# Kernel tuning notes

Hardware: AMD Instinct MI355X
Metric: run time of the kernel (lower is better)

Reference implementation:

```python
import jax, jax.numpy as jnp
import numpy as np


def setup_inputs() -> dict:
    key = jax.random.key(0)
    k1, k2, k3, k4 = jax.random.split(key, 4)
    B, T, IN, D = 32, 256, 64, 128
    x = jax.random.normal(k1, (B, T, IN), dtype=jnp.float32)
    h0 = jnp.zeros((B, D), dtype=jnp.float32)
    Wx = jax.random.normal(k2, (IN, D), dtype=jnp.float32) * 0.01
    Wgate = jax.random.normal(k3, (D, D), dtype=jnp.float32) * 0.01
    Wh = jax.random.normal(k4, (D, D), dtype=jnp.float32) * 0.01
    return {"x": x, "h0": h0, "Wx": Wx, "Wgate": Wgate, "Wh": Wh}


def reference(x, h0, Wx, Wgate, Wh):
    # x: (B, T, in_dim); h0: (B, dim); returns (h_final, y, hidden_grads, dh_dWh)
    def step_single(h_r, x_r):
        # per-sample gated update: h_r (dim,), x_r (in_dim,)
        pre = x_r @ Wx + h_r @ Wh
        a = jax.nn.gelu(pre, approximate=False)  # torch GELU() is the exact erf variant
        g = jax.nn.sigmoid(a @ Wgate)
        hn = g * h_r + (1.0 - g)
        return hn, hn

    # per-step, per-sample Jacobian d h_new / d h  (mirrors vmap(jacrev(..., argnums=1)))
    jac_batched = jax.vmap(jax.jacrev(step_single, argnums=0, has_aux=True))

    def body(h, x_t):  # h: (B, dim), x_t: (B, in_dim)
        jac, h_new = jac_batched(h, x_t)  # jac: (B, dim, dim)
        return h_new, (h_new, jac)

    xt = jnp.swapaxes(x, 0, 1)  # (T, B, in_dim)
    h_final, (ys, jacs) = jax.lax.scan(body, h0, xt)
    y = jnp.swapaxes(ys, 0, 1)  # (B, T, dim)

    # last-step Jacobian wrt Wh, evaluated with the post-update h (as in the torch code)
    x_last = x[:, -1, :]

    def f_wh(Wh_):
        pre = x_last @ Wx + h_final @ Wh_
        a = jax.nn.gelu(pre, approximate=False)
        g = jax.nn.sigmoid(a @ Wgate)
        return g * h_final + (1.0 - g)

    dh_dWh = jax.jacrev(f_wh)(Wh)  # (B, dim, dim, dim)
    return (h_final, y, jacs, dh_dWh)
```

## Files before the change

kernel.cpp:

```cpp
#include <hip/hip_runtime.h>


#define JACOFF 1052672L
#define DHWOFF 135270400L

typedef __attribute__((ext_vector_type(8))) short frag_ab;
typedef __attribute__((ext_vector_type(4))) float frag_cd;

__device__ __forceinline__ short f2bf(float f) {
    unsigned u = __builtin_bit_cast(unsigned, f);
    unsigned r = (u + 0x7fffu + ((u >> 16) & 1u)) >> 16;
    return (short)r;
}

__device__ __forceinline__ void wg_barrier() {
    asm volatile("s_waitcnt lgkmcnt(0)\n\ts_barrier" ::: "memory");
}

__device__ __forceinline__ float row_reduce16(float x) {
    int t;
    t = __builtin_amdgcn_mov_dpp(__builtin_bit_cast(int, x), 0x128, 0xF, 0xF, true);
    x += __builtin_bit_cast(float, t);
    t = __builtin_amdgcn_mov_dpp(__builtin_bit_cast(int, x), 0x124, 0xF, 0xF, true);
    x += __builtin_bit_cast(float, t);
    t = __builtin_amdgcn_mov_dpp(__builtin_bit_cast(int, x), 0x4E, 0xF, 0xF, true);
    x += __builtin_bit_cast(float, t);
    t = __builtin_amdgcn_mov_dpp(__builtin_bit_cast(int, x), 0xB1, 0xF, 0xF, true);
    x += __builtin_bit_cast(float, t);
    return x;
}

__device__ __forceinline__ void gelu_pair(float pre, float& a, float& dval) {
    const float inv_sqrt2   = 0.70710678118654752f;
    const float inv_sqrt2pi = 0.39894228040143268f;
    float ex2 = __expf(-0.5f * pre * pre);
    float az  = fabsf(pre) * inv_sqrt2;
    float t   = 1.0f / (1.0f + 0.3275911f * az);
    float poly = ((((1.061405429f * t - 1.453152027f) * t + 1.421413741f) * t
                   - 0.284496736f) * t + 0.254829592f) * t;
    float erf_abs = 1.0f - poly * ex2;
    float erf_z = (pre < 0.f) ? -erf_abs : erf_abs;
    float cdf = 0.5f * (1.0f + erf_z);
    a = pre * cdf;
    dval = cdf + pre * inv_sqrt2pi * ex2;
}

__global__ __launch_bounds__(256) void prep_xw_kernel(
    const float* __restrict__ Wh, const float* __restrict__ Wg,
    const float* __restrict__ x, const float* __restrict__ Wx,
    float* __restrict__ whT, float* __restrict__ wgT, float* __restrict__ xw)
{
    int blk = blockIdx.x;
    int tid = threadIdx.x;
    if (blk < 128) {
        int idx = blk * 256 + tid;
        if (idx < 16384) {
            int k = idx >> 7, i = idx & 127;
            whT[i * 128 + k] = Wh[idx];
        } else {
            int r = idx - 16384;
            int k = r >> 7, i = r & 127;
            wgT[i * 128 + k] = Wg[r];
        }
        return;
    }
    __shared__ float xs[2][64];
    int sub = tid >> 7;
    int bt = (blk - 128) * 2 + sub;
    int i = tid & 127;
    if (i < 64) xs[sub][i] = x[bt * 64 + i];
    __syncthreads();
    float acc = 0.f;
#pragma unroll
    for (int m = 0; m < 64; ++m)
        acc += xs[sub][m] * Wx[m * 128 + i];
    xw[bt * 128 + i] = acc;
}

__global__ __launch_bounds__(512, 1) void scan_pk_kernel(
    const float* __restrict__ xw, const float* __restrict__ h0,
    const float* __restrict__ whT, const float* __restrict__ wgT,
    const float* __restrict__ Wgate, const float* __restrict__ Wh,
    float* __restrict__ out,
    short* __restrict__ Abf, float* __restrict__ wgv, float* __restrict__ wc,
    float* __restrict__ wdF, float* __restrict__ wuF, float* __restrict__ whF,
    short* __restrict__ PT)
{
    int tid = threadIdx.x;
    if (blockIdx.x >= 32) {
        int c = (blockIdx.x - 32) * 32 + (tid >> 4);
        int k0 = (tid & 15) * 8;
        int i = c >> 7, j = c & 127;
        short v[8];
#pragma unroll
        for (int m = 0; m < 8; ++m) {
            float wg = Wgate[(k0 + m) * 128 + i];
            float wh = Wh[j * 128 + k0 + m];
            v[m] = f2bf(wg * wh);
        }
        *(frag_ab*)(PT + (long)c * 128 + k0) = *(frag_ab*)v;
        return;
    }

    const int b = blockIdx.x;
    const int og = tid >> 4;
    const int kg = tid & 15;
    const int mm = kg & 3;
    const int iw = og * 4 + kg;
    const bool wlane = (kg < 4);

    __shared__ float hbuf[2][128];
    __shared__ float abuf[128];

    float wh[4][8], wgc[4][8];
#pragma unroll
    for (int m = 0; m < 4; ++m) {
        const float* whr = whT + (og * 4 + m) * 128 + kg * 8;
        const float* wgr = wgT + (og * 4 + m) * 128 + kg * 8;
        float4 a4 = *(const float4*)(whr);
        float4 b4 = *(const float4*)(whr + 4);
        wh[m][0] = a4.x; wh[m][1] = a4.y; wh[m][2] = a4.z; wh[m][3] = a4.w;
        wh[m][4] = b4.x; wh[m][5] = b4.y; wh[m][6] = b4.z; wh[m][7] = b4.w;
        float4 c4 = *(const float4*)(wgr);
        float4 d4 = *(const float4*)(wgr + 4);
        wgc[m][0] = c4.x; wgc[m][1] = c4.y; wgc[m][2] = c4.z; wgc[m][3] = c4.w;
        wgc[m][4] = d4.x; wgc[m][5] = d4.y; wgc[m][6] = d4.z; wgc[m][7] = d4.w;
    }
    if (wlane) hbuf[0][iw] = h0[b * 128 + iw];
    __syncthreads();

    float4 xwv4 = *(const float4*)(xw + (b * 256 + 0) * 128 + og * 4);
    float4 xw14 = *(const float4*)(xw + (b * 256 + 1) * 128 + og * 4);

    for (int t = 0; t < 256; ++t) {
        int p = t & 1;
        int tn = (t < 254) ? t + 2 : 255;
        float4 xw24 = *(const float4*)(xw + (b * 256 + tn) * 128 + og * 4);

        float h8[8];
        {
            const float* hb = &hbuf[p][kg * 8];
            float4 a4 = *(const float4*)(hb);
            float4 b4 = *(const float4*)(hb + 4);
            h8[0] = a4.x; h8[1] = a4.y; h8[2] = a4.z; h8[3] = a4.w;
            h8[4] = b4.x; h8[5] = b4.y; h8[6] = b4.z; h8[7] = b4.w;
        }
        float s0 = 0.f, s1 = 0.f, s2 = 0.f, s3 = 0.f;
#pragma unroll
        for (int kk = 0; kk < 8; ++kk) {
            s0 += h8[kk] * wh[0][kk];
            s1 += h8[kk] * wh[1][kk];
            s2 += h8[kk] * wh[2][kk];
            s3 += h8[kk] * wh[3][kk];
        }
        s0 = row_reduce16(s0); s1 = row_reduce16(s1);
        s2 = row_reduce16(s2); s3 = row_reduce16(s3);

        float pre = (mm == 0) ? (xwv4.x + s0) : (mm == 1) ? (xwv4.y + s1)
                  : (mm == 2) ? (xwv4.z + s2) : (xwv4.w + s3);
        float a, dval;
        gelu_pair(pre, a, dval);

        long tb = (long)(t * 32 + b) * 128 + iw;
        if (wlane) {
            Abf[tb] = f2bf(dval);
            abuf[iw] = a;
        }
        wg_barrier();

        float a8[8];
        {
            const float* ab = &abuf[kg * 8];
            float4 a4 = *(const float4*)(ab);
            float4 b4 = *(const float4*)(ab + 4);
            a8[0] = a4.x; a8[1] = a4.y; a8[2] = a4.z; a8[3] = a4.w;
            a8[4] = b4.x; a8[5] = b4.y; a8[6] = b4.z; a8[7] = b4.w;
        }
        float r0 = 0.f, r1 = 0.f, r2 = 0.f, r3 = 0.f;
#pragma unroll
        for (int kk = 0; kk < 8; ++kk) {
            r0 += a8[kk] * wgc[0][kk];
            r1 += a8[kk] * wgc[1][kk];
            r2 += a8[kk] * wgc[2][kk];
            r3 += a8[kk] * wgc[3][kk];
        }
        r0 = row_reduce16(r0); r1 = row_reduce16(r1);
        r2 = row_reduce16(r2); r3 = row_reduce16(r3);
        float r = (mm == 0) ? r0 : (mm == 1) ? r1 : (mm == 2) ? r2 : r3;

        float g = 1.0f / (1.0f + __expf(-r));
        float hp = hbuf[p][og * 4 + mm];
        float c = (hp - 1.0f) * g * (1.0f - g);
        float hn = g * hp + 1.0f - g;
        if (wlane) {
            hbuf[p ^ 1][iw] = hn;
            wgv[tb] = g;
            wc[tb] = c;
            out[4096 + (b * 256 + t) * 128 + iw] = hn;
        }
        xwv4 = xw14; xw14 = xw24;
        wg_barrier();
    }

    float hfin = hbuf[0][og * 4 + mm];
    if (wlane) {
        out[b * 128 + iw] = hbuf[0][iw];
        whF[b * 128 + iw] = hbuf[0][iw];
    }

    {
        float h8[8];
        {
            const float* hb = &hbuf[0][kg * 8];
            float4 a4 = *(const float4*)(hb);
            float4 b4 = *(const float4*)(hb + 4);
            h8[0] = a4.x; h8[1] = a4.y; h8[2] = a4.z; h8[3] = a4.w;
            h8[4] = b4.x; h8[5] = b4.y; h8[6] = b4.z; h8[7] = b4.w;
        }
        float s0 = 0.f, s1 = 0.f, s2 = 0.f, s3 = 0.f;
#pragma unroll
        for (int kk = 0; kk < 8; ++kk) {
            s0 += h8[kk] * wh[0][kk];
            s1 += h8[kk] * wh[1][kk];
            s2 += h8[kk] * wh[2][kk];
            s3 += h8[kk] * wh[3][kk];
        }
        s0 = row_reduce16(s0); s1 = row_reduce16(s1);
        s2 = row_reduce16(s2); s3 = row_reduce16(s3);
        float pre = (mm == 0) ? (xwv4.x + s0) : (mm == 1) ? (xwv4.y + s1)
                  : (mm == 2) ? (xwv4.z + s2) : (xwv4.w + s3);
        float a, dval;
        gelu_pair(pre, a, dval);
        if (wlane) {
            wdF[b * 128 + iw] = dval;
            abuf[iw] = a;
        }
        __syncthreads();
        float a8[8];
        {
            const float* ab = &abuf[kg * 8];
            float4 a4 = *(const float4*)(ab);
            float4 b4 = *(const float4*)(ab + 4);
            a8[0] = a4.x; a8[1] = a4.y; a8[2] = a4.z; a8[3] = a4.w;
            a8[4] = b4.x; a8[5] = b4.y; a8[6] = b4.z; a8[7] = b4.w;
        }
        float r0 = 0.f, r1 = 0.f, r2 = 0.f, r3 = 0.f;
#pragma unroll
        for (int kk = 0; kk < 8; ++kk) {
            r0 += a8[kk] * wgc[0][kk];
            r1 += a8[kk] * wgc[1][kk];
            r2 += a8[kk] * wgc[2][kk];
            r3 += a8[kk] * wgc[3][kk];
        }
        r0 = row_reduce16(r0); r1 = row_reduce16(r1);
        r2 = row_reduce16(r2); r3 = row_reduce16(r3);
        float r = (mm == 0) ? r0 : (mm == 1) ? r1 : (mm == 2) ? r2 : r3;
        float g = 1.0f / (1.0f + __expf(-r));
        if (wlane) wuF[b * 128 + iw] = (hfin - 1.0f) * g * (1.0f - g);
    }
}

__global__ __launch_bounds__(256) void jacmm_dhdw_kernel(
    const short* __restrict__ Abf,
    const short* __restrict__ PT,
    const float* __restrict__ wgv,
    const float* __restrict__ wc,
    const float* __restrict__ Wgate,
    const float* __restrict__ dF, const float* __restrict__ uF, const float* __restrict__ hF,
    float* __restrict__ out)
{
    int bx = blockIdx.x;
    int tid = threadIdx.x;
    int grp = bx / 3, rem = bx % 3;

    __shared__ float cstage[64 * 132];

    if (rem == 2) {
        __shared__ float hs[128], dsh[128];
        int b = grp >> 7, i = grp & 127;
        if (tid < 128) {
            hs[tid] = hF[b * 128 + tid];
            dsh[tid] = dF[b * 128 + tid];
        }
        __syncthreads();
        float u = uF[b * 128 + i];
        int q0 = (tid & 31) * 4, p0 = (tid >> 5) * 16;
        float w0 = u * dsh[q0 + 0] * Wgate[(q0 + 0) * 128 + i];
        float w1 = u * dsh[q0 + 1] * Wgate[(q0 + 1) * 128 + i];
        float w2 = u * dsh[q0 + 2] * Wgate[(q0 + 2) * 128 + i];
        float w3 = u * dsh[q0 + 3] * Wgate[(q0 + 3) * 128 + i];
        float* dst = out + DHWOFF + (long)grp * 16384;
#pragma unroll
        for (int pp = 0; pp < 16; ++pp) {
            float hp = hs[p0 + pp];
            frag_cd v4; v4[0] = hp * w0; v4[1] = hp * w1; v4[2] = hp * w2; v4[3] = hp * w3;
            __builtin_nontemporal_store(v4, (frag_cd*)(dst + (p0 + pp) * 128 + q0));
        }
        return;
    }

    int jb = grp * 2 + rem;
    int rb = jb & 63;
    int cb = jb >> 6;

    const short* Ag = Abf + (long)rb * (128 * 128);
    const short* Bg = PT + (long)cb * (128 * 128);

    int w = tid >> 6;
    int lane = tid & 63;
    int wr = w >> 1;
    int wcol = w & 1;
    int lrow = lane & 15;
    int quad = lane >> 4;

    long rowbase = (long)rb * 128;
    float ci[4][4], gi[4][4];
#pragma unroll
    for (int p = 0; p < 4; ++p) {
        int trow0 = wr * 64 + p * 16 + quad * 4;
#pragma unroll
        for (int reg = 0; reg < 4; ++reg) {
            long row = rowbase + trow0 + reg;
            ci[p][reg] = wc[row * 128 + cb];
            gi[p][reg] = wgv[row * 128 + cb];
        }
    }

    frag_cd acc[4][4];
#pragma unroll
    for (int p = 0; p < 4; ++p)
#pragma unroll
        for (int q = 0; q < 4; ++q) {
            acc[p][q][0] = 0.f; acc[p][q][1] = 0.f; acc[p][q][2] = 0.f; acc[p][q][3] = 0.f;
        }

#pragma unroll
    for (int kk = 0; kk < 4; ++kk) {
        int ko8 = (kk * 4 + quad) * 8;
        frag_ab af[4], bf[4];
#pragma unroll
        for (int p = 0; p < 4; ++p) {
            int r = wr * 64 + p * 16 + lrow;
            af[p] = *(const frag_ab*)(Ag + r * 128 + ko8);
        }
#pragma unroll
        for (int q = 0; q < 4; ++q) {
            int n = wcol * 64 + q * 16 + lrow;
            bf[q] = *(const frag_ab*)(Bg + n * 128 + ko8);
        }
#pragma unroll
        for (int p = 0; p < 4; ++p)
#pragma unroll
            for (int q = 0; q < 4; ++q)
                acc[p][q] = __builtin_amdgcn_mfma_f32_16x16x32_bf16(af[p], bf[q], acc[p][q], 0, 0, 0);
    }

#pragma unroll
    for (int p0 = 0; p0 < 4; p0 += 2) {
        if (p0) __syncthreads();
#pragma unroll
        for (int dp = 0; dp < 2; ++dp) {
            int p = p0 + dp;
#pragma unroll
            for (int reg = 0; reg < 4; ++reg) {
                int lr = wr * 32 + dp * 16 + quad * 4 + reg;
                float cval = ci[p][reg], gval = gi[p][reg];
#pragma unroll
                for (int q = 0; q < 4; ++q) {
                    int tcol = wcol * 64 + q * 16 + lrow;
                    float v = cval * acc[p][q][reg];
                    if (tcol == cb) v += gval;
                    cstage[lr * 132 + tcol] = v;
                }
            }
        }
        __syncthreads();
        int col4 = (tid & 31) * 4;
        int rg = tid >> 5;
#pragma unroll
        for (int rr = 0; rr < 8; ++rr) {
            int lr = rg * 8 + rr;
            int grow = (lr < 32) ? (p0 * 16 + lr) : (64 + p0 * 16 + (lr - 32));
            frag_cd v4 = *(const frag_cd*)&cstage[lr * 132 + col4];
            __builtin_nontemporal_store(
                v4, (frag_cd*)(out + JACOFF + (rowbase + grow) * 16384 + (long)cb * 128 + col4));
        }
    }
}

extern "C" void kernel_launch(void* const* d_in, const int* in_sizes, int n_in,
                              void* d_out, int out_size, void* d_ws, size_t ws_size,
                              hipStream_t stream)
{
    (void)in_sizes; (void)n_in; (void)out_size; (void)ws_size;
    const float* x     = (const float*)d_in[0];
    const float* h0    = (const float*)d_in[1];
    const float* Wx    = (const float*)d_in[2];
    const float* Wgate = (const float*)d_in[3];
    const float* Wh    = (const float*)d_in[4];
    float* out = (float*)d_out;
    float* ws  = (float*)d_ws;

    float* xw  = ws;
    float* whT = ws + 1048576;
    float* wgT = ws + 1064960;
    float* wgv = ws + 1081344;
    float* wc  = ws + 2129920;
    float* wdF = ws + 3178496;
    float* wuF = ws + 3182592;
    float* whF = ws + 3186688;
    short* Abf = (short*)(ws + 3190784);
    short* PT  = (short*)(ws + 3715072);

    prep_xw_kernel<<<4224, 256, 0, stream>>>(Wh, Wgate, x, Wx, whT, wgT, xw);
    scan_pk_kernel<<<544, 512, 0, stream>>>(xw, h0, whT, wgT, Wgate, Wh, out,
                                            Abf, wgv, wc, wdF, wuF, whF, PT);
    jacmm_dhdw_kernel<<<12288, 256, 0, stream>>>(Abf, PT, wgv, wc, Wgate, wdF, wuF, whF, out);
}
```

Before: 1.046 ms.

## Fuse scan and Jacobian GEMM into a persistent kernel with progress flags

Merges the sequential scan and the Jacobian/dh_dWh writer into one persistent kernel. 32 blocks run the recurrence and publish per-16-step progress counters, while the other blocks take work tickets from an atomic counter and spin until the timesteps they need are ready. The Jacobian GEMM can then overlap with the latency-bound scan instead of waiting for it to finish. The PT bf16 product precompute moves into the prep kernel. This adds spin-wait and atomic ticketing costs, uses relaxed atomics for producer-consumer ordering, and relies on all 256 blocks being co-resident.

```diff
diff --git a/kernel.cpp b/kernel.cpp
--- a/kernel.cpp
+++ b/kernel.cpp
@@ -3,6 +3,9 @@
 
 #define JACOFF 1052672L
 #define DHWOFF 135270400L
+
+#define NTICK_JAC   8192u
+#define NTICK_TOTAL 10240u
 
 typedef __attribute__((ext_vector_type(8))) short frag_ab;
 typedef __attribute__((ext_vector_type(4))) float frag_cd;
@@ -45,10 +48,11 @@
     dval = cdf + pre * inv_sqrt2pi * ex2;
 }
 
-__global__ __launch_bounds__(256) void prep_xw_kernel(
+__global__ __launch_bounds__(256) void prep_kernel(
     const float* __restrict__ Wh, const float* __restrict__ Wg,
     const float* __restrict__ x, const float* __restrict__ Wx,
-    float* __restrict__ whT, float* __restrict__ wgT, float* __restrict__ xw)
+    float* __restrict__ whT, float* __restrict__ wgT, float* __restrict__ xw,
+    short* __restrict__ PT, unsigned* __restrict__ ctrl)
 {
     int blk = blockIdx.x;
     int tid = threadIdx.x;
@@ -64,327 +68,349 @@
         }
         return;
     }
-    __shared__ float xs[2][64];
-    int sub = tid >> 7;
-    int bt = (blk - 128) * 2 + sub;
-    int i = tid & 127;
-    if (i < 64) xs[sub][i] = x[bt * 64 + i];
-    __syncthreads();
-    float acc = 0.f;
-#pragma unroll
-    for (int m = 0; m < 64; ++m)
-        acc += xs[sub][m] * Wx[m * 128 + i];
-    xw[bt * 128 + i] = acc;
-}
-
-__global__ __launch_bounds__(512, 1) void scan_pk_kernel(
+    if (blk < 4224) {
+        __shared__ float xs[2][64];
+        int sub = tid >> 7;
+        int bt = (blk - 128) * 2 + sub;
+        int i = tid & 127;
+        if (i < 64) xs[sub][i] = x[bt * 64 + i];
+        __syncthreads();
+        float acc = 0.f;
+#pragma unroll
+        for (int m = 0; m < 64; ++m)
+            acc += xs[sub][m] * Wx[m * 128 + i];
+        xw[bt * 128 + i] = acc;
+        return;
+    }
+    if (blk < 5248) {
+        int c = (blk - 4224) * 16 + (tid >> 4);
+        int k0 = (tid & 15) * 8;
+        int i = c >> 7, j = c & 127;
+        short v[8];
+#pragma unroll
+        for (int m = 0; m < 8; ++m) {
+            float wg = Wg[(k0 + m) * 128 + i];
+            float wh = Wh[j * 128 + k0 + m];
+            v[m] = f2bf(wg * wh);
+        }
+        *(frag_ab*)(PT + (long)c * 128 + k0) = *(frag_ab*)v;
+        return;
+    }
+    if (tid < 128) ctrl[tid] = 0u;
+}
+
+__global__ __launch_bounds__(512, 1) void fused_kernel(
     const float* __restrict__ xw, const float* __restrict__ h0,
     const float* __restrict__ whT, const float* __restrict__ wgT,
-    const float* __restrict__ Wgate, const float* __restrict__ Wh,
+    const float* __restrict__ Wgate,
     float* __restrict__ out,
     short* __restrict__ Abf, float* __restrict__ wgv, float* __restrict__ wc,
     float* __restrict__ wdF, float* __restrict__ wuF, float* __restrict__ whF,
-    short* __restrict__ PT)
+    const short* __restrict__ PT, unsigned* __restrict__ ctrl)
 {
-    int tid = threadIdx.x;
-    if (blockIdx.x >= 32) {
-        int c = (blockIdx.x - 32) * 32 + (tid >> 4);
-        int k0 = (tid & 15) * 8;
-        int i = c >> 7, j = c & 127;
-        short v[8];
-#pragma unroll
-        for (int m = 0; m < 8; ++m) {
-            float wg = Wgate[(k0 + m) * 128 + i];
-            float wh = Wh[j * 128 + k0 + m];
-            v[m] = f2bf(wg * wh);
-        }
-        *(frag_ab*)(PT + (long)c * 128 + k0) = *(frag_ab*)v;
-        return;
-    }
-
-    const int b = blockIdx.x;
-    const int og = tid >> 4;
-    const int kg = tid & 15;
-    const int mm = kg & 3;
-    const int iw = og * 4 + kg;
-    const bool wlane = (kg < 4);
-
+    const int tid = threadIdx.x;
     __shared__ float hbuf[2][128];
     __shared__ float abuf[128];
-
-    float wh[4][8], wgc[4][8];
-#pragma unroll
-    for (int m = 0; m < 4; ++m) {
-        const float* whr = whT + (og * 4 + m) * 128 + kg * 8;
-        const float* wgr = wgT + (og * 4 + m) * 128 + kg * 8;
-        float4 a4 = *(const float4*)(whr);
-        float4 b4 = *(const float4*)(whr + 4);
-        wh[m][0] = a4.x; wh[m][1] = a4.y; wh[m][2] = a4.z; wh[m][3] = a4.w;
-        wh[m][4] = b4.x; wh[m][5] = b4.y; wh[m][6] = b4.z; wh[m][7] = b4.w;
-        float4 c4 = *(const float4*)(wgr);
-        float4 d4 = *(const float4*)(wgr + 4);
-        wgc[m][0] = c4.x; wgc[m][1] = c4.y; wgc[m][2] = c4.z; wgc[m][3] = c4.w;
-        wgc[m][4] = d4.x; wgc[m][5] = d4.y; wgc[m][6] = d4.z; wgc[m][7] = d4.w;
+    __shared__ float cstage[64 * 132];
+    __shared__ float hs2[2][128], ds2[2][128];
+    __shared__ unsigned sh_u;
+
+    if (blockIdx.x < 32) {
+        const int b = blockIdx.x;
+        const int og = tid >> 4;
+        const int kg = tid & 15;
+        const int mm = kg & 3;
+        const int iw = og * 4 + kg;
+        const bool wlane = (kg < 4);
+
+        float wh[4][8], wgc[4][8];
+#pragma unroll
+        for (int m = 0; m < 4; ++m) {
+            const float* whr = whT + (og * 4 + m) * 128 + kg * 8;
+            const float* wgr = wgT + (og * 4 + m) * 128 + kg * 8;
+            float4 a4 = *(const float4*)(whr);
+            float4 b4 = *(const float4*)(whr + 4);
+            wh[m][0] = a4.x; wh[m][1] = a4.y; wh[m][2] = a4.z; wh[m][3] = a4.w;
+            wh[m][4] = b4.x; wh[m][5] = b4.y; wh[m][6] = b4.z; wh[m][7] = b4.w;
+            float4 c4 = *(const float4*)(wgr);
+            float4 d4 = *(const float4*)(wgr + 4);
+            wgc[m][0] = c4.x; wgc[m][1] = c4.y; wgc[m][2] = c4.z; wgc[m][3] = c4.w;
+            wgc[m][4] = d4.x; wgc[m][5] = d4.y; wgc[m][6] = d4.z; wgc[m][7] = d4.w;
+        }
+        if (wlane) hbuf[0][iw] = h0[b * 128 + iw];
+        __syncthreads();
+
+        float4 xwv4 = *(const float4*)(xw + (b * 256 + 0) * 128 + og * 4);
+        float4 xw14 = *(const float4*)(xw + (b * 256 + 1) * 128 + og * 4);
+
+        for (int t = 0; t < 256; ++t) {
+            int p = t & 1;
+            int tn = (t < 254) ? t + 2 : 255;
+            float4 xw24 = *(const float4*)(xw + (b * 256 + tn) * 128 + og * 4);
+
+            float h8[8];
+            {
+                const float* hb = &hbuf[p][kg * 8];
+                float4 a4 = *(const float4*)(hb);
+                float4 b4 = *(const float4*)(hb + 4);
+                h8[0] = a4.x; h8[1] = a4.y; h8[2] = a4.z; h8[3] = a4.w;
+                h8[4] = b4.x; h8[5] = b4.y; h8[6] = b4.z; h8[7] = b4.w;
+            }
+            float s0 = 0.f, s1 = 0.f, s2 = 0.f, s3 = 0.f;
+#pragma unroll
+            for (int kk = 0; kk < 8; ++kk) {
+                s0 += h8[kk] * wh[0][kk];
+                s1 += h8[kk] * wh[1][kk];
+                s2 += h8[kk] * wh[2][kk];
+                s3 += h8[kk] * wh[3][kk];
+            }
+            s0 = row_reduce16(s0); s1 = row_reduce16(s1);
+            s2 = row_reduce16(s2); s3 = row_reduce16(s3);
+            float pre = (mm == 0) ? (xwv4.x + s0) : (mm == 1) ? (xwv4.y + s1)
+                      : (mm == 2) ? (xwv4.z + s2) : (xwv4.w + s3);
+            float a, dval;
+            gelu_pair(pre, a, dval);
+
+            long tb = (long)(t * 32 + b) * 128 + iw;
+            if (wlane) {
+                __hip_atomic_store(&Abf[tb], f2bf(dval), __ATOMIC_RELAXED, __HIP_MEMORY_SCOPE_AGENT);
+                abuf[iw] = a;
+            }
+            wg_barrier();
+
+            float a8[8];
+            {
+                const float* ab = &abuf[kg * 8];
+                float4 a4 = *(const float4*)(ab);
+                float4 b4 = *(const float4*)(ab + 4);
+                a8[0] = a4.x; a8[1] = a4.y; a8[2] = a4.z; a8[3] = a4.w;
+                a8[4] = b4.x; a8[5] = b4.y; a8[6] = b4.z; a8[7] = b4.w;
+            }
+            float r0 = 0.f, r1 = 0.f, r2 = 0.f, r3 = 0.f;
+#pragma unroll
+            for (int kk = 0; kk < 8; ++kk) {
+                r0 += a8[kk] * wgc[0][kk];
+                r1 += a8[kk] * wgc[1][kk];
+                r2 += a8[kk] * wgc[2][kk];
+                r3 += a8[kk] * wgc[3][kk];
+            }
+            r0 = row_reduce16(r0); r1 = row_reduce16(r1);
+            r2 = row_reduce16(r2); r3 = row_reduce16(r3);
+            float r = (mm == 0) ? r0 : (mm == 1) ? r1 : (mm == 2) ? r2 : r3;
+
+            float g = 1.0f / (1.0f + __expf(-r));
+            float hp = hbuf[p][og * 4 + mm];
+            float c = (hp - 1.0f) * g * (1.0f - g);
+            float hn = g * hp + 1.0f - g;
+            if (wlane) {
+                hbuf[p ^ 1][iw] = hn;
+                __hip_atomic_store(&wgv[tb], g, __ATOMIC_RELAXED, __HIP_MEMORY_SCOPE_AGENT);
+                __hip_atomic_store(&wc[tb], c, __ATOMIC_RELAXED, __HIP_MEMORY_SCOPE_AGENT);
+                out[4096 + (b * 256 + t) * 128 + iw] = hn;
+            }
+            xwv4 = xw14; xw14 = xw24;
+            if ((t & 15) == 15) {
+                __syncthreads();
+                if (tid == 0)
+                    __hip_atomic_fetch_add(&ctrl[t >> 4], 1u, __ATOMIC_RELAXED, __HIP_MEMORY_SCOPE_AGENT);
+            } else {
+                wg_barrier();
+            }
+        }
+
+        float hfin = hbuf[0][og * 4 + mm];
+        if (wlane) {
+            out[b * 128 + iw] = hbuf[0][iw];
+            __hip_atomic_store(&whF[b * 128 + iw], hbuf[0][iw], __ATOMIC_RELAXED, __HIP_MEMORY_SCOPE_AGENT);
+        }
+
+        {
+            float h8[8];
+            {
+                const float* hb = &hbuf[0][kg * 8];
+                float4 a4 = *(const float4*)(hb);
+                float4 b4 = *(const float4*)(hb + 4);
+                h8[0] = a4.x; h8[1] = a4.y; h8[2] = a4.z; h8[3] = a4.w;
+                h8[4] = b4.x; h8[5] = b4.y; h8[6] = b4.z; h8[7] = b4.w;
+            }
+            float s0 = 0.f, s1 = 0.f, s2 = 0.f, s3 = 0.f;
+#pragma unroll
+            for (int kk = 0; kk < 8; ++kk) {
+                s0 += h8[kk] * wh[0][kk];
+                s1 += h8[kk] * wh[1][kk];
+                s2 += h8[kk] * wh[2][kk];
+                s3 += h8[kk] * wh[3][kk];
+            }
+            s0 = row_reduce16(s0); s1 = row_reduce16(s1);
+            s2 = row_reduce16(s2); s3 = row_reduce16(s3);
+            float pre = (mm == 0) ? (xwv4.x + s0) : (mm == 1) ? (xwv4.y + s1)
+                      : (mm == 2) ? (xwv4.z + s2) : (xwv4.w + s3);
+            float a, dval;
+            gelu_pair(pre, a, dval);
+            if (wlane) {
+                __hip_atomic_store(&wdF[b * 128 + iw], dval, __ATOMIC_RELAXED, __HIP_MEMORY_SCOPE_AGENT);
+                abuf[iw] = a;
+            }
+            __syncthreads();
+            float a8[8];
+            {
+                const float* ab = &abuf[kg * 8];
+                float4 a4 = *(const float4*)(ab);
+                float4 b4 = *(const float4*)(ab + 4);
+                a8[0] = a4.x; a8[1] = a4.y; a8[2] = a4.z; a8[3] = a4.w;
+                a8[4] = b4.x; a8[5] = b4.y; a8[6] = b4.z; a8[7] = b4.w;
+            }
+            float r0 = 0.f, r1 = 0.f, r2 = 0.f, r3 = 0.f;
+#pragma unroll
+            for (int kk = 0; kk < 8; ++kk) {
+                r0 += a8[kk] * wgc[0][kk];
+                r1 += a8[kk] * wgc[1][kk];
+                r2 += a8[kk] * wgc[2][kk];
+                r3 += a8[kk] * wgc[3][kk];
+            }
+            r0 = row_reduce16(r0); r1 = row_reduce16(r1);
+            r2 = row_reduce16(r2); r3 = row_reduce16(r3);
+            float r = (mm == 0) ? r0 : (mm == 1) ? r1 : (mm == 2) ? r2 : r3;
+            float g = 1.0f / (1.0f + __expf(-r));
+            if (wlane)
+                __hip_atomic_store(&wuF[b * 128 + iw], (hfin - 1.0f) * g * (1.0f - g),
+                                   __ATOMIC_RELAXED, __HIP_MEMORY_SCOPE_AGENT);
+        }
+        __syncthreads();
+        if (tid == 0)
+            __hip_atomic_fetch_add(&ctrl[16], 1u, __ATOMIC_RELAXED, __HIP_MEMORY_SCOPE_AGENT);
     }
-    if (wlane) hbuf[0][iw] = h0[b * 128 + iw];
-    __syncthreads();
-
-    float4 xwv4 = *(const float4*)(xw + (b * 256 + 0) * 128 + og * 4);
-    float4 xw14 = *(const float4*)(xw + (b * 256 + 1) * 128 + og * 4);
-
-    for (int t = 0; t < 256; ++t) {
-        int p = t & 1;
-        int tn = (t < 254) ? t + 2 : 255;
-        float4 xw24 = *(const float4*)(xw + (b * 256 + tn) * 128 + og * 4);
-
-        float h8[8];
-        {
-            const float* hb = &hbuf[p][kg * 8];
-            float4 a4 = *(const float4*)(hb);
-            float4 b4 = *(const float4*)(hb + 4);
-            h8[0] = a4.x; h8[1] = a4.y; h8[2] = a4.z; h8[3] = a4.w;
-            h8[4] = b4.x; h8[5] = b4.y; h8[6] = b4.z; h8[7] = b4.w;
-        }
-        float s0 = 0.f, s1 = 0.f, s2 = 0.f, s3 = 0.f;
-#pragma unroll
-        for (int kk = 0; kk < 8; ++kk) {
-            s0 += h8[kk] * wh[0][kk];
-            s1 += h8[kk] * wh[1][kk];
-            s2 += h8[kk] * wh[2][kk];
-            s3 += h8[kk] * wh[3][kk];
-        }
-        s0 = row_reduce16(s0); s1 = row_reduce16(s1);
-        s2 = row_reduce16(s2); s3 = row_reduce16(s3);
-
-        float pre = (mm == 0) ? (xwv4.x + s0) : (mm == 1) ? (xwv4.y + s1)
-                  : (mm == 2) ? (xwv4.z + s2) : (xwv4.w + s3);
-        float a, dval;
-        gelu_pair(pre, a, dval);
-
-        long tb = (long)(t * 32 + b) * 128 + iw;
-        if (wlane) {
-            Abf[tb] = f2bf(dval);
-            abuf[iw] = a;
-        }
-        wg_barrier();
-
-        float a8[8];
-        {
-            const float* ab = &abuf[kg * 8];
-            float4 a4 = *(const float4*)(ab);
-            float4 b4 = *(const float4*)(ab + 4);
-            a8[0] = a4.x; a8[1] = a4.y; a8[2] = a4.z; a8[3] = a4.w;
-            a8[4] = b4.x; a8[5] = b4.y; a8[6] = b4.z; a8[7] = b4.w;
-        }
-        float r0 = 0.f, r1 = 0.f, r2 = 0.f, r3 = 0.f;
-#pragma unroll
-        for (int kk = 0; kk < 8; ++kk) {
-            r0 += a8[kk] * wgc[0][kk];
-            r1 += a8[kk] * wgc[1][kk];
-            r2 += a8[kk] * wgc[2][kk];
-            r3 += a8[kk] * wgc[3][kk];
-        }
-        r0 = row_reduce16(r0); r1 = row_reduce16(r1);
-        r2 = row_reduce16(r2); r3 = row_reduce16(r3);
-        float r = (mm == 0) ? r0 : (mm == 1) ? r1 : (mm == 2) ? r2 : r3;
-
-        float g = 1.0f / (1.0f + __expf(-r));
-        float hp = hbuf[p][og * 4 + mm];
-        float c = (hp - 1.0f) * g * (1.0f - g);
-        float hn = g * hp + 1.0f - g;
-        if (wlane) {
-            hbuf[p ^ 1][iw] = hn;
-            wgv[tb] = g;
-            wc[tb] = c;
-            out[4096 + (b * 256 + t) * 128 + iw] = hn;
-        }
-        xwv4 = xw14; xw14 = xw24;
-        wg_barrier();
-    }
-
-    float hfin = hbuf[0][og * 4 + mm];
-    if (wlane) {
-        out[b * 128 + iw] = hbuf[0][iw];
-        whF[b * 128 + iw] = hbuf[0][iw];
-    }
-
-    {
-        float h8[8];
-        {
-            const float* hb = &hbuf[0][kg * 8];
-            float4 a4 = *(const float4*)(hb);
-            float4 b4 = *(const float4*)(hb + 4);
-            h8[0] = a4.x; h8[1] = a4.y; h8[2] = a4.z; h8[3] = a4.w;
-            h8[4] = b4.x; h8[5] = b4.y; h8[6] = b4.z; h8[7] = b4.w;
-        }
-        float s0 = 0.f, s1 = 0.f, s2 = 0.f, s3 = 0.f;
-#pragma unroll
-        for (int kk = 0; kk < 8; ++kk) {
-            s0 += h8[kk] * wh[0][kk];
-            s1 += h8[kk] * wh[1][kk];
-            s2 += h8[kk] * wh[2][kk];
-            s3 += h8[kk] * wh[3][kk];
-        }
-        s0 = row_reduce16(s0); s1 = row_reduce16(s1);
-        s2 = row_reduce16(s2); s3 = row_reduce16(s3);
-        float pre = (mm == 0) ? (xwv4.x + s0) : (mm == 1) ? (xwv4.y + s1)
-                  : (mm == 2) ? (xwv4.z + s2) : (xwv4.w + s3);
-        float a, dval;
-        gelu_pair(pre, a, dval);
-        if (wlane) {
-            wdF[b * 128 + iw] = dval;
-            abuf[iw] = a;
-        }
+
+    const int lane = tid & 63;
+    for (;;) {
+        if (tid == 0)
+            sh_u = __hip_atomic_fetch_add(&ctrl[64], 1u, __ATOMIC_RELAXED, __HIP_MEMORY_SCOPE_AGENT);
         __syncthreads();
-        float a8[8];
-        {
-            const float* ab = &abuf[kg * 8];
-            float4 a4 = *(const float4*)(ab);
-            float4 b4 = *(const float4*)(ab + 4);
-            a8[0] = a4.x; a8[1] = a4.y; a8[2] = a4.z; a8[3] = a4.w;
-            a8[4] = b4.x; a8[5] = b4.y; a8[6] = b4.z; a8[7] = b4.w;
-        }
-        float r0 = 0.f, r1 = 0.f, r2 = 0.f, r3 = 0.f;
-#pragma unroll
-        for (int kk = 0; kk < 8; ++kk) {
-            r0 += a8[kk] * wgc[0][kk];
-            r1 += a8[kk] * wgc[1][kk];
-            r2 += a8[kk] * wgc[2][kk];
-            r3 += a8[kk] * wgc[3][kk];
-        }
-        r0 = row_reduce16(r0); r1 = row_reduce16(r1);
-        r2 = row_reduce16(r2); r3 = row_reduce16(r3);
-        float r = (mm == 0) ? r0 : (mm == 1) ? r1 : (mm == 2) ? r2 : r3;
-        float g = 1.0f / (1.0f + __expf(-r));
-        if (wlane) wuF[b * 128 + iw] = (hfin - 1.0f) * g * (1.0f - g);
-    }
-}
-
-__global__ __launch_bounds__(256) void jacmm_dhdw_kernel(
-    const short* __restrict__ Abf,
-    const short* __restrict__ PT,
-    const float* __restrict__ wgv,
-    const float* __restrict__ wc,
-    const float* __restrict__ Wgate,
-    const float* __restrict__ dF, const float* __restrict__ uF, const float* __restrict__ hF,
-    float* __restrict__ out)
-{
-    int bx = blockIdx.x;
-    int tid = threadIdx.x;
-    int grp = bx / 3, rem = bx % 3;
-
-    __shared__ float cstage[64 * 132];
-
-    if (rem == 2) {
-        __shared__ float hs[128], dsh[128];
-        int b = grp >> 7, i = grp & 127;
-        if (tid < 128) {
-            hs[tid] = hF[b * 128 + tid];
-            dsh[tid] = dF[b * 128 + tid];
+        unsigned u = sh_u;
+        if (u >= NTICK_TOTAL) break;
+
+        if (u < NTICK_JAC) {
+            int rb = (int)(u >> 7), cb = (int)(u & 127u);
+            int fidx = (4 * rb + 3) >> 4;
+            if (tid == 0) {
+                while (__hip_atomic_load(&ctrl[fidx], __ATOMIC_RELAXED, __HIP_MEMORY_SCOPE_AGENT) < 32u)
+                    __builtin_amdgcn_s_sleep(32);
+            }
+            __syncthreads();
+
+            const short* Ag = Abf + (long)rb * (128 * 128);
+            const short* Bg = PT + (long)cb * (128 * 128);
+
+            int w = tid >> 6;
+            int wr = w >> 2;
+            int wcol = w & 3;
+            int lrow = lane & 15;
+            int quad = lane >> 4;
+
+            long rowbase = (long)rb * 128;
+            float ci[4][4], gi[4][4];
+#pragma unroll
+            for (int p = 0; p < 4; ++p) {
+                int trow0 = wr * 64 + p * 16 + quad * 4;
+#pragma unroll
+                for (int reg = 0; reg < 4; ++reg) {
+                    long row = rowbase + trow0 + reg;
+                    ci[p][reg] = wc[row * 128 + cb];
+                    gi[p][reg] = wgv[row * 128 + cb];
+                }
+            }
+
+            frag_cd acc[4][2];
+#pragma unroll
+            for (int p = 0; p < 4; ++p)
+#pragma unroll
+                for (int q = 0; q < 2; ++q) {
+                    acc[p][q][0] = 0.f; acc[p][q][1] = 0.f; acc[p][q][2] = 0.f; acc[p][q][3] = 0.f;
+                }
+
+#pragma unroll
+            for (int kk = 0; kk < 4; ++kk) {
+                int ko8 = (kk * 4 + quad) * 8;
+                frag_ab af[4], bf2[2];
+#pragma unroll
+                for (int p = 0; p < 4; ++p) {
+                    int r = wr * 64 + p * 16 + lrow;
+                    af[p] = *(const frag_ab*)(Ag + r * 128 + ko8);
+                }
+#pragma unroll
+                for (int q = 0; q < 2; ++q) {
+                    int n = wcol * 32 + q * 16 + lrow;
+                    bf2[q] = *(const frag_ab*)(Bg + n * 128 + ko8);
+                }
+#pragma unroll
+                for (int p = 0; p < 4; ++p)
+#pragma unroll
+                    for (int q = 0; q < 2; ++q)
+                        acc[p][q] = __builtin_amdgcn_mfma_f32_16x16x32_bf16(af[p], bf2[q], acc[p][q], 0, 0, 0);
+            }
+
+#pragma unroll
+            for (int p0 = 0; p0 < 4; p0 += 2) {
+                if (p0) __syncthreads();
+#pragma unroll
+                for (int dp = 0; dp < 2; ++dp) {
+                    int p = p0 + dp;
+#pragma unroll
+                    for (int reg = 0; reg < 4; ++reg) {
+                        int lr = wr * 32 + dp * 16 + quad * 4 + reg;
+                        float cval = ci[p][reg], gval = gi[p][reg];
+#pragma unroll
+                        for (int q = 0; q < 2; ++q) {
+                            int tcol = wcol * 32 + q * 16 + lrow;
+                            float v = cval * acc[p][q][reg];
+                            if (tcol == cb) v += gval;
+                            cstage[lr * 132 + tcol] = v;
+                        }
+                    }
+                }
+                __syncthreads();
+                int col4 = (tid & 31) * 4;
+                int rgp = tid >> 5;
+#pragma unroll
+                for (int rr = 0; rr < 4; ++rr) {
+                    int lr = rgp * 4 + rr;
+                    int grow = (lr < 32) ? (p0 * 16 + lr) : (64 + p0 * 16 + (lr - 32));
+                    frag_cd v4 = *(const frag_cd*)&cstage[lr * 132 + col4];
+                    __builtin_nontemporal_store(
+                        v4, (frag_cd*)(out + JACOFF + (rowbase + grow) * 16384 + (long)cb * 128 + col4));
+                }
+            }
+        } else {
+            if (tid == 0) {
+                while (__hip_atomic_load(&ctrl[16], __ATOMIC_RELAXED, __HIP_MEMORY_SCOPE_AGENT) < 32u)
+                    __builtin_amdgcn_s_sleep(32);
+            }
+            __syncthreads();
+
+            int v = (int)(u - NTICK_JAC);
+            int half = tid >> 8, t2 = tid & 255;
+            int gu = v * 2 + half;
+            int b = gu >> 7, ii = gu & 127;
+            if (t2 < 128) {
+                hs2[half][t2] = whF[b * 128 + t2];
+                ds2[half][t2] = wdF[b * 128 + t2];
+            }
+            __syncthreads();
+            float u_ = wuF[b * 128 + ii];
+            int q0 = (t2 & 31) * 4, p0 = (t2 >> 5) * 16;
+            float w0 = u_ * ds2[half][q0 + 0] * Wgate[(q0 + 0) * 128 + ii];
+            float w1 = u_ * ds2[half][q0 + 1] * Wgate[(q0 + 1) * 128 + ii];
+            float w2 = u_ * ds2[half][q0 + 2] * Wgate[(q0 + 2) * 128 + ii];
+            float w3 = u_ * ds2[half][q0 + 3] * Wgate[(q0 + 3) * 128 + ii];
+            float* dst = out + DHWOFF + (long)gu * 16384;
+#pragma unroll
+            for (int pp = 0; pp < 16; ++pp) {
+                float hp = hs2[half][p0 + pp];
+                frag_cd v4; v4[0] = hp * w0; v4[1] = hp * w1; v4[2] = hp * w2; v4[3] = hp * w3;
+                __builtin_nontemporal_store(v4, (frag_cd*)(dst + (p0 + pp) * 128 + q0));
+            }
         }
         __syncthreads();
-        float u = uF[b * 128 + i];
-        int q0 = (tid & 31) * 4, p0 = (tid >> 5) * 16;
-        float w0 = u * dsh[q0 + 0] * Wgate[(q0 + 0) * 128 + i];
-        float w1 = u * dsh[q0 + 1] * Wgate[(q0 + 1) * 128 + i];
-        float w2 = u * dsh[q0 + 2] * Wgate[(q0 + 2) * 128 + i];
-        float w3 = u * dsh[q0 + 3] * Wgate[(q0 + 3) * 128 + i];
-        float* dst = out + DHWOFF + (long)grp * 16384;
-#pragma unroll
-        for (int pp = 0; pp < 16; ++pp) {
-            float hp = hs[p0 + pp];
-            frag_cd v4; v4[0] = hp * w0; v4[1] = hp * w1; v4[2] = hp * w2; v4[3] = hp * w3;
-            __builtin_nontemporal_store(v4, (frag_cd*)(dst + (p0 + pp) * 128 + q0));
-        }
-        return;
-    }
-
-    int jb = grp * 2 + rem;
-    int rb = jb & 63;
-    int cb = jb >> 6;
-
-    const short* Ag = Abf + (long)rb * (128 * 128);
-    const short* Bg = PT + (long)cb * (128 * 128);
-
-    int w = tid >> 6;
-    int lane = tid & 63;
-    int wr = w >> 1;
-    int wcol = w & 1;
-    int lrow = lane & 15;
-    int quad = lane >> 4;
-
-    long rowbase = (long)rb * 128;
-    float ci[4][4], gi[4][4];
-#pragma unroll
-    for (int p = 0; p < 4; ++p) {
-        int trow0 = wr * 64 + p * 16 + quad * 4;
-#pragma unroll
-        for (int reg = 0; reg < 4; ++reg) {
-            long row = rowbase + trow0 + reg;
-            ci[p][reg] = wc[row * 128 + cb];
-            gi[p][reg] = wgv[row * 128 + cb];
-        }
-    }
-
-    frag_cd acc[4][4];
-#pragma unroll
-    for (int p = 0; p < 4; ++p)
-#pragma unroll
-        for (int q = 0; q < 4; ++q) {
-            acc[p][q][0] = 0.f; acc[p][q][1] = 0.f; acc[p][q][2] = 0.f; acc[p][q][3] = 0.f;
-        }
-
-#pragma unroll
-    for (int kk = 0; kk < 4; ++kk) {
-        int ko8 = (kk * 4 + quad) * 8;
-        frag_ab af[4], bf[4];
-#pragma unroll
-        for (int p = 0; p < 4; ++p) {
-            int r = wr * 64 + p * 16 + lrow;
-            af[p] = *(const frag_ab*)(Ag + r * 128 + ko8);
-        }
-#pragma unroll
-        for (int q = 0; q < 4; ++q) {
-            int n = wcol * 64 + q * 16 + lrow;
-            bf[q] = *(const frag_ab*)(Bg + n * 128 + ko8);
-        }
-#pragma unroll
-        for (int p = 0; p < 4; ++p)
-#pragma unroll
-            for (int q = 0; q < 4; ++q)
-                acc[p][q] = __builtin_amdgcn_mfma_f32_16x16x32_bf16(af[p], bf[q], acc[p][q], 0, 0, 0);
-    }
-
-#pragma unroll
-    for (int p0 = 0; p0 < 4; p0 += 2) {
-        if (p0) __syncthreads();
-#pragma unroll
-        for (int dp = 0; dp < 2; ++dp) {
-            int p = p0 + dp;
-#pragma unroll
-            for (int reg = 0; reg < 4; ++reg) {
-                int lr = wr * 32 + dp * 16 + quad * 4 + reg;
-                float cval = ci[p][reg], gval = gi[p][reg];
-#pragma unroll
-                for (int q = 0; q < 4; ++q) {
-                    int tcol = wcol * 64 + q * 16 + lrow;
-                    float v = cval * acc[p][q][reg];
-                    if (tcol == cb) v += gval;
-                    cstage[lr * 132 + tcol] = v;
-                }
-            }
-        }
-        __syncthreads();
-        int col4 = (tid & 31) * 4;
-        int rg = tid >> 5;
-#pragma unroll
-        for (int rr = 0; rr < 8; ++rr) {
-            int lr = rg * 8 + rr;
-            int grow = (lr < 32) ? (p0 * 16 + lr) : (64 + p0 * 16 + (lr - 32));
-            frag_cd v4 = *(const frag_cd*)&cstage[lr * 132 + col4];
-            __builtin_nontemporal_store(
-                v4, (frag_cd*)(out + JACOFF + (rowbase + grow) * 16384 + (long)cb * 128 + col4));
-        }
     }
 }
 
@@ -411,9 +437,9 @@
     float* whF = ws + 3186688;
     short* Abf = (short*)(ws + 3190784);
     short* PT  = (short*)(ws + 3715072);
-
-    prep_xw_kernel<<<4224, 256, 0, stream>>>(Wh, Wgate, x, Wx, whT, wgT, xw);
-    scan_pk_kernel<<<544, 512, 0, stream>>>(xw, h0, whT, wgT, Wgate, Wh, out,
-                                            Abf, wgv, wc, wdF, wuF, whF, PT);
-    jacmm_dhdw_kernel<<<12288, 256, 0, stream>>>(Abf, PT, wgv, wc, Wgate, wdF, wuF, whF, out);
-}
+    unsigned* ctrl = (unsigned*)(ws + 4763648);
+
+    prep_kernel<<<5249, 256, 0, stream>>>(Wh, Wgate, x, Wx, whT, wgT, xw, PT, ctrl);
+    fused_kernel<<<256, 512, 53248, stream>>>(xw, h0, whT, wgT, Wgate, out,
+                                              Abf, wgv, wc, wdF, wuF, whF, PT, ctrl);
+}
```

Result: faster. 1.007 ms (-3.8%).
